# Optimization experiments

Measured on AMD Instinct MI355X. Metric: run time of the kernel, lower is better.

## Reference

```python
import jax, jax.numpy as jnp
import numpy as np
from jax import lax

INPUT, HIDDEN, OUT = 5, 32, 2

def setup_inputs() -> dict:
    key = jax.random.key(0)
    ks = jax.random.split(key, 7)
    s_ih = 1.0 / np.sqrt(HIDDEN)
    return {
        "x": jax.random.normal(ks[0], (16384, 200, INPUT), dtype=jnp.float32),
        "W_ih": jax.random.uniform(ks[1], (4 * HIDDEN, INPUT), jnp.float32, -s_ih, s_ih),
        "W_hh": jax.random.uniform(ks[2], (4 * HIDDEN, HIDDEN), jnp.float32, -s_ih, s_ih),
        "b_ih": jax.random.uniform(ks[3], (4 * HIDDEN,), jnp.float32, -s_ih, s_ih),
        "b_hh": jax.random.uniform(ks[4], (4 * HIDDEN,), jnp.float32, -s_ih, s_ih),
        "W_fc": jax.random.uniform(ks[5], (OUT, HIDDEN), jnp.float32, -s_ih, s_ih),
        "b_fc": jax.random.uniform(ks[6], (OUT,), jnp.float32, -s_ih, s_ih),
    }

def reference(x, W_ih, W_hh, b_ih, b_hh, W_fc, b_fc):
    B = x.shape[0]
    # Precompute input projections for all timesteps in one GEMM: [B,T,4H]
    x_proj = jnp.einsum("bti,gi->btg", x, W_ih) + (b_ih + b_hh)
    xs = jnp.swapaxes(x_proj, 0, 1)  # [T, B, 4H]

    def step(carry, xg):
        h, c = carry
        gates = xg + h @ W_hh.T  # [B, 4H]
        i, f, g, o = jnp.split(gates, 4, axis=-1)  # torch gate order i,f,g,o
        i = jax.nn.sigmoid(i)
        f = jax.nn.sigmoid(f)
        g = jnp.tanh(g)
        o = jax.nn.sigmoid(o)
        c = f * c + i * g
        h = o * jnp.tanh(c)
        return (h, c), None

    h0 = jnp.zeros((B, HIDDEN), x.dtype)
    c0 = jnp.zeros((B, HIDDEN), x.dtype)
    (h_n, _), _ = lax.scan(step, (h0, c0), xs)
    return h_n @ W_fc.T + b_fc  # [B, 2]
```

## Files before the change

kernel.cpp:

```cpp
#include <hip/hip_runtime.h>


typedef __bf16 bf16x8 __attribute__((ext_vector_type(8)));
typedef float  f32x4  __attribute__((ext_vector_type(4)));
typedef unsigned int u32;

constexpr int kT = 200, kIN = 5, kH = 32;
constexpr int CT = 40;

constexpr float kL  = 1.4426950408889634f;
constexpr float k2L = 2.8853900817779268f;

union FragU { bf16x8 v; __bf16 b[8]; unsigned short s[8]; u32 u[4]; uint4 q4; };

__device__ __forceinline__ unsigned short bfbits(__bf16 b) {
    union { __bf16 b; unsigned short s; } u; u.b = b; return u.s;
}
__device__ __forceinline__ void split2(float x, __bf16& hi, __bf16& lo) {
    hi = (__bf16)x;
    lo = (__bf16)(x - (float)hi);
}

__global__ __launch_bounds__(64) void lstm_reg5(
    const float* __restrict__ x,
    const float* __restrict__ W_ih,
    const float* __restrict__ W_hh,
    const float* __restrict__ b_ih,
    const float* __restrict__ b_hh,
    const float* __restrict__ W_fc,
    const float* __restrict__ b_fc,
    float* __restrict__ out)
{
    __shared__ uint4 xbuf[CT][34];

    const int lane = threadIdx.x;
    const int n16  = lane & 15;
    const int q    = lane >> 4;
    const int b0   = blockIdx.x * 16;

    bf16x8 whhA_h[8], whhA_l[8], wihA[8];
#pragma unroll
    for (int t8 = 0; t8 < 8; ++t8) {
        const int g  = t8 & 3, hb = t8 >> 2;
        const int R  = g * 32 + 8 * (n16 >> 2) + 4 * hb + (n16 & 3);
        const float sc = (g == 2) ? k2L : kL;
        FragU H, L;
#pragma unroll
        for (int j = 0; j < 8; ++j)
            split2(sc * W_hh[R * kH + q * 8 + j], H.b[j], L.b[j]);
        whhA_h[t8] = H.v; whhA_l[t8] = L.v;

        float wr[5];
#pragma unroll
        for (int i = 0; i < 5; ++i) wr[i] = sc * W_ih[R * kIN + i];
        __bf16 bh, bl;
        split2(sc * (b_ih[R] + b_hh[R]), bh, bl);

        FragU F;
        F.u[0] = F.u[1] = F.u[2] = F.u[3] = 0u;
        if (q == 0) {
#pragma unroll
            for (int i = 0; i < 5; ++i) F.b[i] = (__bf16)wr[i];
#pragma unroll
            for (int i = 0; i < 3; ++i) F.b[5 + i] = (__bf16)wr[i];
        } else if (q == 1) {
            F.b[0] = (__bf16)wr[3];
            F.b[1] = (__bf16)wr[4];
#pragma unroll
            for (int i = 0; i < 5; ++i) {
                __bf16 hbb, lbb; split2(wr[i], hbb, lbb);
                F.b[2 + i] = lbb;
            }
            F.b[7] = bh;
        } else if (q == 2) {
            F.b[0] = bl;
        }
        wihA[t8] = F.v;
    }

    for (int t2 = lane; t2 < CT; t2 += 64) {
        xbuf[t2][32] = make_uint4(0x3F80u, 0u, 0u, 0u);
        xbuf[t2][33] = make_uint4(0u, 0u, 0u, 0u);
    }

    const int col = (q < 2) ? (n16 * 2 + q) : (30 + q);
    const f32x4 zf4 = {0.f, 0.f, 0.f, 0.f};

    float c8[8] = {0.f, 0.f, 0.f, 0.f, 0.f, 0.f, 0.f, 0.f};
    FragU Bh, Bl;
    Bh.u[0] = Bh.u[1] = Bh.u[2] = Bh.u[3] = 0u;
    Bl.u[0] = Bl.u[1] = Bl.u[2] = Bl.u[3] = 0u;

    for (int phase = 0; phase < kT / CT; ++phase) {
        {
            const int mm = lane >> 2, pp = lane & 3;
            const float2* xr2 = (const float2*)(x + (size_t)(b0 + mm) * (kT * kIN)
                                                  + (size_t)(phase * CT + pp * 10) * kIN);
            float xv[50];
#pragma unroll
            for (int i = 0; i < 25; ++i) {
                float2 v = xr2[i];
                xv[2 * i] = v.x; xv[2 * i + 1] = v.y;
            }
#pragma unroll
            for (int s5 = 0; s5 < 10; ++s5) {
                u32 xh[5], xl[5];
#pragma unroll
                for (int i = 0; i < 5; ++i) {
                    __bf16 hbb, lbb; split2(xv[s5 * 5 + i], hbb, lbb);
                    xh[i] = bfbits(hbb); xl[i] = bfbits(lbb);
                }
                uint4 f0 = make_uint4(xh[0] | (xh[1] << 16),
                                      xh[2] | (xh[3] << 16),
                                      xh[4] | (xl[0] << 16),
                                      xl[1] | (xl[2] << 16));
                uint4 f1 = make_uint4(xl[3] | (xl[4] << 16),
                                      xh[0] | (xh[1] << 16),
                                      xh[2] | (xh[3] << 16),
                                      xh[4] | (0x3F80u << 16));
                const int tc = pp * 10 + s5;
                xbuf[tc][mm * 2 + 0] = f0;
                xbuf[tc][mm * 2 + 1] = f1;
            }
        }
        __syncthreads();

        FragU xg; xg.q4 = xbuf[0][col];

#pragma unroll 1
        for (int tc = 0; tc < CT; ++tc) {
            FragU xgn;
            const int tn = (tc + 1 < CT) ? tc + 1 : 0;
            xgn.q4 = xbuf[tn][col];

            f32x4 acc[8];
#pragma unroll
            for (int t8 = 0; t8 < 8; ++t8) {
                f32x4 a = __builtin_amdgcn_mfma_f32_16x16x32_bf16(wihA[t8], xg.v, zf4, 0, 0, 0);
                a = __builtin_amdgcn_mfma_f32_16x16x32_bf16(whhA_h[t8], Bh.v, a, 0, 0, 0);
                a = __builtin_amdgcn_mfma_f32_16x16x32_bf16(whhA_h[t8], Bl.v, a, 0, 0, 0);
                a = __builtin_amdgcn_mfma_f32_16x16x32_bf16(whhA_l[t8], Bh.v, a, 0, 0, 0);
                acc[t8] = a;
            }

#pragma unroll
            for (int m2 = 0; m2 < 4; ++m2) {
                const int j0 = 2 * m2, j1 = j0 + 1;
                const int hb = j0 >> 2;
                const int r0 = j0 & 3, r1 = j1 & 3;
                float ai0 = acc[hb * 4 + 0][r0], af0 = acc[hb * 4 + 1][r0];
                float ag0 = acc[hb * 4 + 2][r0], ao0 = acc[hb * 4 + 3][r0];
                float ai1 = acc[hb * 4 + 0][r1], af1 = acc[hb * 4 + 1][r1];
                float ag1 = acc[hb * 4 + 2][r1], ao1 = acc[hb * 4 + 3][r1];

                float u0 = __builtin_amdgcn_exp2f(-ai0), v0 = __builtin_amdgcn_exp2f(-ag0);
                float w0 = __builtin_amdgcn_exp2f(-af0), p0 = __builtin_amdgcn_exp2f(-ao0);
                float u1 = __builtin_amdgcn_exp2f(-ai1), v1 = __builtin_amdgcn_exp2f(-ag1);
                float w1 = __builtin_amdgcn_exp2f(-af1), p1 = __builtin_amdgcn_exp2f(-ao1);

                float A0 = (1.0f + u0) * (1.0f + v0);
                float A1 = (1.0f + u1) * (1.0f + v1);
                float B0 = 1.0f + w0, B1 = 1.0f + w1;
                float rA = __builtin_amdgcn_rcpf(A0 * A1);
                float rB = __builtin_amdgcn_rcpf(B0 * B1);

                float t0 = fmaf(v0, -k2L, k2L);
                float t1 = fmaf(v1, -k2L, k2L);
                float c0 = fmaf(c8[j0], B1 * rB, t0 * (A1 * rA));
                float c1 = fmaf(c8[j1], B0 * rB, t1 * (A0 * rA));
                c0 = fmaxf(c0, -35.0f);
                c1 = fmaxf(c1, -35.0f);
                c8[j0] = c0; c8[j1] = c1;

                float s0 = __builtin_amdgcn_exp2f(-c0);
                float s1 = __builtin_amdgcn_exp2f(-c1);
                float C0 = (1.0f + p0) * (1.0f + s0);
                float C1 = (1.0f + p1) * (1.0f + s1);
                float rC = __builtin_amdgcn_rcpf(C0 * C1);
                float h0 = (1.0f - s0) * (C1 * rC);
                float h1 = (1.0f - s1) * (C0 * rC);

                split2(h0, Bh.b[j0], Bl.b[j0]);
                split2(h1, Bh.b[j1], Bl.b[j1]);
            }

            xg = xgn;
        }
    }

    __syncthreads();
    float* hfin = (float*)xbuf;
#pragma unroll
    for (int jj = 0; jj < 8; ++jj)
        hfin[n16 * 33 + q * 8 + jj] = (float)Bh.b[jj] + (float)Bl.b[jj];
    __syncthreads();
    if (lane < 32) {
        const int m = lane >> 1, o = lane & 1;
        float s = b_fc[o];
#pragma unroll
        for (int j = 0; j < kH; ++j)
            s = fmaf(hfin[m * 33 + j], W_fc[o * kH + j], s);
        out[(size_t)(b0 + m) * 2 + o] = s;
    }
}

extern "C" void kernel_launch(void* const* d_in, const int* in_sizes, int n_in,
                              void* d_out, int out_size, void* d_ws, size_t ws_size,
                              hipStream_t stream) {
    const float* x    = (const float*)d_in[0];
    const float* W_ih = (const float*)d_in[1];
    const float* W_hh = (const float*)d_in[2];
    const float* b_ih = (const float*)d_in[3];
    const float* b_hh = (const float*)d_in[4];
    const float* W_fc = (const float*)d_in[5];
    const float* b_fc = (const float*)d_in[6];
    float* out = (float*)d_out;

    hipLaunchKernelGGL(lstm_reg5, dim3(1024), dim3(64), 0, stream,
                       x, W_ih, W_hh, b_ih, b_hh, W_fc, b_fc, out);
}
```

Baseline: 245.4 us.

## Hoist input-projection MFMAs off recurrence critical path and overlap exp with MFMAs

The input-projection MFMA for the next timestep is now computed after the current step's recurrent MFMAs and carried in an accumulator array. This takes it off the h-dependent critical chain, which drops from four to three dependent MFMAs per gate tile. The recurrent MFMAs are split into two halves so the exp2 work on the first half can overlap the second half's MFMAs. Launch bounds now pin one block per SM, which frees registers for the extra accumulators but may limit occupancy.

New measurement: 259.5 us. 1.06x slower.

```diff
diff --git a/kernel.cpp b/kernel.cpp
--- a/kernel.cpp
+++ b/kernel.cpp
@@ -21,7 +21,7 @@
     lo = (__bf16)(x - (float)hi);
 }
 
-__global__ __launch_bounds__(64) void lstm_reg5(
+__global__ __launch_bounds__(64, 1) void lstm_reg6(
     const float* __restrict__ x,
     const float* __restrict__ W_ih,
     const float* __restrict__ W_hh,
@@ -90,6 +90,8 @@
     FragU Bh, Bl;
     Bh.u[0] = Bh.u[1] = Bh.u[2] = Bh.u[3] = 0u;
     Bl.u[0] = Bl.u[1] = Bl.u[2] = Bl.u[3] = 0u;
+
+    f32x4 accx[8];
 
     for (int phase = 0; phase < kT / CT; ++phase) {
         {
@@ -125,7 +127,12 @@
         }
         __syncthreads();
 
-        FragU xg; xg.q4 = xbuf[0][col];
+        {
+            FragU x0; x0.q4 = xbuf[0][col];
+#pragma unroll
+            for (int t8 = 0; t8 < 8; ++t8)
+                accx[t8] = __builtin_amdgcn_mfma_f32_16x16x32_bf16(wihA[t8], x0.v, zf4, 0, 0, 0);
+        }
 
 #pragma unroll 1
         for (int tc = 0; tc < CT; ++tc) {
@@ -134,29 +141,47 @@
             xgn.q4 = xbuf[tn][col];
 
             f32x4 acc[8];
-#pragma unroll
-            for (int t8 = 0; t8 < 8; ++t8) {
-                f32x4 a = __builtin_amdgcn_mfma_f32_16x16x32_bf16(wihA[t8], xg.v, zf4, 0, 0, 0);
-                a = __builtin_amdgcn_mfma_f32_16x16x32_bf16(whhA_h[t8], Bh.v, a, 0, 0, 0);
+            float eu[8], ew[8], ev[8], ep[8];
+
+#pragma unroll
+            for (int t8 = 0; t8 < 4; ++t8) {
+                f32x4 a = __builtin_amdgcn_mfma_f32_16x16x32_bf16(whhA_h[t8], Bh.v, accx[t8], 0, 0, 0);
                 a = __builtin_amdgcn_mfma_f32_16x16x32_bf16(whhA_h[t8], Bl.v, a, 0, 0, 0);
                 a = __builtin_amdgcn_mfma_f32_16x16x32_bf16(whhA_l[t8], Bh.v, a, 0, 0, 0);
                 acc[t8] = a;
             }
+#pragma unroll
+            for (int j = 0; j < 4; ++j) {
+                eu[j] = __builtin_amdgcn_exp2f(-acc[0][j]);
+                ew[j] = __builtin_amdgcn_exp2f(-acc[1][j]);
+                ev[j] = __builtin_amdgcn_exp2f(-acc[2][j]);
+                ep[j] = __builtin_amdgcn_exp2f(-acc[3][j]);
+            }
+
+#pragma unroll
+            for (int t8 = 4; t8 < 8; ++t8) {
+                f32x4 a = __builtin_amdgcn_mfma_f32_16x16x32_bf16(whhA_h[t8], Bh.v, accx[t8], 0, 0, 0);
+                a = __builtin_amdgcn_mfma_f32_16x16x32_bf16(whhA_h[t8], Bl.v, a, 0, 0, 0);
+                a = __builtin_amdgcn_mfma_f32_16x16x32_bf16(whhA_l[t8], Bh.v, a, 0, 0, 0);
+                acc[t8] = a;
+            }
+#pragma unroll
+            for (int j = 4; j < 8; ++j) {
+                eu[j] = __builtin_amdgcn_exp2f(-acc[4][j - 4]);
+                ew[j] = __builtin_amdgcn_exp2f(-acc[5][j - 4]);
+                ev[j] = __builtin_amdgcn_exp2f(-acc[6][j - 4]);
+                ep[j] = __builtin_amdgcn_exp2f(-acc[7][j - 4]);
+            }
+
+#pragma unroll
+            for (int t8 = 0; t8 < 8; ++t8)
+                accx[t8] = __builtin_amdgcn_mfma_f32_16x16x32_bf16(wihA[t8], xgn.v, zf4, 0, 0, 0);
 
 #pragma unroll
             for (int m2 = 0; m2 < 4; ++m2) {
                 const int j0 = 2 * m2, j1 = j0 + 1;
-                const int hb = j0 >> 2;
-                const int r0 = j0 & 3, r1 = j1 & 3;
-                float ai0 = acc[hb * 4 + 0][r0], af0 = acc[hb * 4 + 1][r0];
-                float ag0 = acc[hb * 4 + 2][r0], ao0 = acc[hb * 4 + 3][r0];
-                float ai1 = acc[hb * 4 + 0][r1], af1 = acc[hb * 4 + 1][r1];
-                float ag1 = acc[hb * 4 + 2][r1], ao1 = acc[hb * 4 + 3][r1];
-
-                float u0 = __builtin_amdgcn_exp2f(-ai0), v0 = __builtin_amdgcn_exp2f(-ag0);
-                float w0 = __builtin_amdgcn_exp2f(-af0), p0 = __builtin_amdgcn_exp2f(-ao0);
-                float u1 = __builtin_amdgcn_exp2f(-ai1), v1 = __builtin_amdgcn_exp2f(-ag1);
-                float w1 = __builtin_amdgcn_exp2f(-af1), p1 = __builtin_amdgcn_exp2f(-ao1);
+                float u0 = eu[j0], v0 = ev[j0], w0 = ew[j0], p0 = ep[j0];
+                float u1 = eu[j1], v1 = ev[j1], w1 = ew[j1], p1 = ep[j1];
 
                 float A0 = (1.0f + u0) * (1.0f + v0);
                 float A1 = (1.0f + u1) * (1.0f + v1);
@@ -183,8 +208,6 @@
                 split2(h0, Bh.b[j0], Bl.b[j0]);
                 split2(h1, Bh.b[j1], Bl.b[j1]);
             }
-
-            xg = xgn;
         }
     }
 
@@ -216,6 +239,6 @@
     const float* b_fc = (const float*)d_in[6];
     float* out = (float*)d_out;
 
-    hipLaunchKernelGGL(lstm_reg5, dim3(1024), dim3(64), 0, stream,
+    hipLaunchKernelGGL(lstm_reg6, dim3(1024), dim3(64), 0, stream,
                        x, W_ih, W_hh, b_ih, b_hh, W_fc, b_fc, out);
 }
```
